# Optimization experiments

Hardware: AMD Instinct MI355X
Metric: run time of the kernel (lower is better)

## Reference

```python
import jax, jax.numpy as jnp
import numpy as np

D_IN = 1024
D_H = 1024

def setup_inputs() -> dict:
    key = jax.random.key(0)
    ks = jax.random.split(key, 9)
    s = 1.0 / np.sqrt(D_IN)
    inp = {
        'x': jax.random.normal(ks[0], (4, 2048, D_IN), dtype=jnp.float32),
        'wq': jax.random.uniform(ks[1], (D_IN, D_H), jnp.float32, -s, s),
        'bq': jax.random.uniform(ks[2], (D_H,), jnp.float32, -s, s),
        'wk': jax.random.uniform(ks[3], (D_IN, D_H), jnp.float32, -s, s),
        'bk': jax.random.uniform(ks[4], (D_H,), jnp.float32, -s, s),
        'wv': jax.random.uniform(ks[5], (D_IN, D_H), jnp.float32, -s, s),
        'bv': jax.random.uniform(ks[6], (D_H,), jnp.float32, -s, s),
        'wo': jax.random.uniform(ks[7], (D_H, D_IN), jnp.float32, -s, s),
        'bo': jax.random.uniform(ks[8], (D_IN,), jnp.float32, -s, s),
    }
    return inp

def reference(x, wq, bq, wk, bk, wv, bv, wo, bo):
    # q,k,v: [b, s, d]
    q = x @ wq + bq
    k = x @ wk + bk
    v = x @ wv + bv
    scale = 1.0 / jnp.sqrt(jnp.asarray(D_H, x.dtype))
    attn = jnp.einsum('bqd,bkd->bqk', q, k) * scale  # [b, s, s]
    attn = jax.nn.softmax(attn, axis=-1)
    score = jnp.einsum('bqk,bkd->bqd', attn, v)
    out = score @ wo + bo
    return out
```

## Files before the change

### kernel.cpp

```cpp
#include <hip/hip_runtime.h>


typedef unsigned short u16;
typedef short bf16x8 __attribute__((ext_vector_type(8)));
typedef float f32x4 __attribute__((ext_vector_type(4)));

#define SEQ 2048
#define DIM 1024

__device__ __forceinline__ u16 f2bf(float f) {
    unsigned u = __builtin_bit_cast(unsigned, f);
    u += 0x7fffu + ((u >> 16) & 1u);
    return (u16)(u >> 16);
}

__device__ __forceinline__ void async16(void* lds, const void* gmem) {
    __builtin_amdgcn_global_load_lds(
        (const __attribute__((address_space(1))) void*)gmem,
        (__attribute__((address_space(3))) void*)lds, 16, 0, 0);
}

__global__ __launch_bounds__(256) void cast_x_kernel(
    const float* __restrict__ x, u16* __restrict__ xb,
    const float* __restrict__ bq, const float* __restrict__ bk,
    const float* __restrict__ bv, float* __restrict__ bqkv,
    float* __restrict__ l)
{
    const int b = blockIdx.x;
    if (b < 8192) {
        const int idx = b * 256 + threadIdx.x;
        float4 v = ((const float4*)x)[idx];
        ushort4 o;
        o.x = f2bf(v.x); o.y = f2bf(v.y); o.z = f2bf(v.z); o.w = f2bf(v.w);
        ((ushort4*)xb)[idx] = o;
    } else {
        const int i = (b - 8192) * 256 + threadIdx.x;
        if (i < 3072)
            bqkv[i] = (i < 1024) ? bq[i] : (i < 2048) ? bk[i - 1024] : bv[i - 2048];
        else if (i < 3072 + 8192)
            l[i - 3072] = 0.f;
    }
}

__global__ __launch_bounds__(256) void transpose_cast_all(
    const float* __restrict__ W0, const float* __restrict__ W1,
    const float* __restrict__ W2, const float* __restrict__ W3,
    u16* __restrict__ Tqkv, u16* __restrict__ To)
{
    __shared__ float tile[32][33];
    const int z = blockIdx.z;
    const float* W = (z == 0) ? W0 : (z == 1) ? W1 : (z == 2) ? W2 : W3;
    u16* T = (z < 3) ? (Tqkv + (size_t)z * 1048576) : To;

    const int bx = blockIdx.x * 32, by = blockIdx.y * 32;
    const int tx = threadIdx.x, ty = threadIdx.y;
    #pragma unroll
    for (int r = 0; r < 4; ++r)
        tile[ty + r * 8][tx] = W[(size_t)(by + ty + r * 8) * DIM + bx + tx];
    __syncthreads();
    #pragma unroll
    for (int r = 0; r < 4; ++r) {
        const float v = tile[tx][ty + r * 8];
        T[(size_t)(bx + ty + r * 8) * DIM + by + tx] = f2bf(v);
    }
}

#define EPI_BF16BIAS 0
#define EPI_BF16     1
#define EPI_ELOGIT   2
#define EPI_PVOUT    3

#define FENCE() asm volatile("" ::: "memory")

#define MFMA_QUAD(mh, nh)                                                    \
    do {                                                                     \
        __builtin_amdgcn_s_setprio(1);                                       \
        _Pragma("unroll")                                                    \
        for (int ks = 0; ks < 2; ++ks)                                       \
            _Pragma("unroll")                                                \
            for (int q = 0; q < 4; ++q)                                      \
                _Pragma("unroll")                                            \
                for (int nn = 0; nn < 2; ++nn)                               \
                    acc[(mh) * 4 + q][(nh) * 2 + nn] =                       \
                        __builtin_amdgcn_mfma_f32_16x16x32_bf16(             \
                            aF[q][ks], bF[(nh) * 2 + nn][ks],                \
                            acc[(mh) * 4 + q][(nh) * 2 + nn], 0, 0, 0);      \
        __builtin_amdgcn_s_setprio(0);                                       \
    } while (0)

template<int EPI, int K, int LDA, int LDB, int LDC>
__global__ __launch_bounds__(512, 2) void gemm8w(
    const u16* __restrict__ A, const u16* __restrict__ Bt,
    const float* __restrict__ bias, u16* __restrict__ C,
    float* __restrict__ Cf, float* __restrict__ lsum,
    float scale, long sA, long sB, long sC)
{
    __shared__ u16 lds[2][2][2][8192];

    constexpr int NT = K / 64;

    const int z = blockIdx.z;
    A  += (size_t)z * sA;
    Bt += (size_t)z * sB;

    const int t = threadIdx.x;
    const int wid = t >> 6, lane = t & 63;
    const int wm = wid >> 2, wn = wid & 3;
    const int lrow = lane & 15, quad = lane >> 4;
    const int m0 = blockIdx.y * 256, n0 = blockIdx.x * 256;

    int ldsoff[2], offA[2], offB[2];
    #pragma unroll
    for (int p = 0; p < 2; ++p) {
        const int L  = p * 8192 + wid * 1024 + lane * 16;
        const int sL = L ^ (((L >> 7) & 7) << 4);
        const int r  = sL >> 7;
        const int c  = (sL & 127) >> 1;
        ldsoff[p] = L;
        offA[p]   = r * LDA + c;
        offB[p]   = r * LDB + c;
    }
    const u16* ABase = A  + (size_t)m0 * LDA;
    const u16* BBase = Bt + (size_t)n0 * LDB;

    auto stage = [&](int tile, int sel) {
        const int mat = sel >> 1, half = sel & 1, buf = tile & 1;
        char* dst = (char*)&lds[buf][mat][half][0];
        const int k0 = tile * 64;
        #pragma unroll
        for (int p = 0; p < 2; ++p) {
            const u16* src = mat
                ? BBase + (size_t)half * (128 * (size_t)LDB) + k0 + offB[p]
                : ABase + (size_t)half * (128 * (size_t)LDA) + k0 + offA[p];
            async16(dst + ldsoff[p], src);
        }
    };

    f32x4 acc[8][4];
    #pragma unroll
    for (int i = 0; i < 8; ++i)
        #pragma unroll
        for (int j = 0; j < 4; ++j)
            acc[i][j] = (f32x4){0.f, 0.f, 0.f, 0.f};

    bf16x8 aF[4][2], bF[4][2];

    auto ldA1 = [&](int buf, int mi, int ks) -> bf16x8 {
        int b = (mi * 16 + lrow) * 128 + ks * 64 + quad * 16;
        b ^= ((b >> 7) & 7) << 4;
        return *(const bf16x8*)((const char*)&lds[buf][0][wm][0] + b);
    };
    auto ldB1 = [&](int buf, int ni, int ks) -> bf16x8 {
        int b = ((wn & 1) * 64 + ni * 16 + lrow) * 128 + ks * 64 + quad * 16;
        b ^= ((b >> 7) & 7) << 4;
        return *(const bf16x8*)((const char*)&lds[buf][1][wn >> 1][0] + b);
    };

    stage(0, 0); stage(0, 1); stage(0, 2); stage(0, 3);
    stage(1, 2); stage(1, 3); stage(1, 0);
    asm volatile("s_waitcnt vmcnt(6)" ::: "memory");
    __builtin_amdgcn_s_barrier();

    #pragma unroll 1
    for (int T = 0; T < NT; ++T) {
        const int buf = T & 1;
        const bool s1 = (T + 1 < NT), s2 = (T + 2 < NT);

        #pragma unroll
        for (int q = 0; q < 4; ++q) {
            aF[q][0] = ldA1(buf, q, 0);
            aF[q][1] = ldA1(buf, q, 1);
        }
        #pragma unroll
        for (int ni = 0; ni < 4; ++ni) {
            bF[ni][0] = ldB1(buf, ni, 0);
            bF[ni][1] = ldB1(buf, ni, 1);
        }
        if (s1) stage(T + 1, 1);
        FENCE(); __builtin_amdgcn_s_barrier();
        MFMA_QUAD(0, 0);
        FENCE(); __builtin_amdgcn_s_barrier();

        MFMA_QUAD(0, 1);
        FENCE(); __builtin_amdgcn_s_barrier();

        #pragma unroll
        for (int q = 0; q < 4; ++q) {
            aF[q][0] = ldA1(buf, 4 + q, 0);
            aF[q][1] = ldA1(buf, 4 + q, 1);
        }
        if (s2) { stage(T + 2, 2); stage(T + 2, 3); }
        FENCE(); __builtin_amdgcn_s_barrier();
        MFMA_QUAD(1, 1);
        FENCE(); __builtin_amdgcn_s_barrier();

        if (s2) {
            stage(T + 2, 0);
            asm volatile("s_waitcnt vmcnt(6)" ::: "memory");
        } else {
            asm volatile("s_waitcnt vmcnt(0)" ::: "memory");
        }
        FENCE(); __builtin_amdgcn_s_barrier();
        MFMA_QUAD(1, 0);
        FENCE(); __builtin_amdgcn_s_barrier();
    }

    if (EPI == EPI_PVOUT) Cf += (size_t)z * sC;
    else                  C  += (size_t)z * sC;

    #pragma unroll
    for (int mi = 0; mi < 8; ++mi) {
        const int row = m0 + wm * 128 + mi * 16 + quad * 4;
        if (EPI == EPI_BF16BIAS) {
            #pragma unroll
            for (int ni = 0; ni < 4; ++ni) {
                const int col = n0 + wn * 64 + ni * 16 + lrow;
                const float bb = bias[col];
                const f32x4 a = acc[mi][ni];
                #pragma unroll
                for (int r = 0; r < 4; ++r)
                    C[(size_t)(row + r) * LDC + col] = f2bf(a[r] + bb);
            }
        } else if (EPI == EPI_BF16) {
            #pragma unroll
            for (int ni = 0; ni < 4; ++ni) {
                const int col = n0 + wn * 64 + ni * 16 + lrow;
                const f32x4 a = acc[mi][ni];
                #pragma unroll
                for (int r = 0; r < 4; ++r)
                    C[(size_t)(row + r) * LDC + col] = f2bf(a[r]);
            }
        } else if (EPI == EPI_ELOGIT) {
            float rs[4] = {0.f, 0.f, 0.f, 0.f};
            #pragma unroll
            for (int ni = 0; ni < 4; ++ni) {
                const int col = n0 + wn * 64 + ni * 16 + lrow;
                const f32x4 a = acc[mi][ni];
                #pragma unroll
                for (int r = 0; r < 4; ++r) {
                    const float e = __expf(a[r] * scale);
                    C[(size_t)(row + r) * LDC + col] = f2bf(e);
                    rs[r] += e;
                }
            }
            #pragma unroll
            for (int r = 0; r < 4; ++r) {
                float s = rs[r];
                s += __shfl_xor(s, 1, 64);
                s += __shfl_xor(s, 2, 64);
                s += __shfl_xor(s, 4, 64);
                s += __shfl_xor(s, 8, 64);
                if (lrow == 0)
                    atomicAdd(&lsum[(size_t)z * 2048 + row + r], s);
            }
        } else {
            float linv[4];
            #pragma unroll
            for (int r = 0; r < 4; ++r)
                linv[r] = 1.0f / lsum[(size_t)z * 2048 + row + r];
            #pragma unroll
            for (int ni = 0; ni < 4; ++ni) {
                const int col = n0 + wn * 64 + ni * 16 + lrow;
                const float bb = bias[col];
                const f32x4 a = acc[mi][ni];
                #pragma unroll
                for (int r = 0; r < 4; ++r)
                    Cf[(size_t)(row + r) * LDC + col] = a[r] * linv[r] + bb;
            }
        }
    }
}

extern "C" void kernel_launch(void* const* d_in, const int* in_sizes, int n_in,
                              void* d_out, int out_size, void* d_ws, size_t ws_size,
                              hipStream_t stream)
{
    const float* x  = (const float*)d_in[0];
    const float* wq = (const float*)d_in[1];
    const float* bq = (const float*)d_in[2];
    const float* wk = (const float*)d_in[3];
    const float* bk = (const float*)d_in[4];
    const float* wv = (const float*)d_in[5];
    const float* bv = (const float*)d_in[6];
    const float* wo = (const float*)d_in[7];
    const float* bo = (const float*)d_in[8];
    float* out = (float*)d_out;

    u16* w16   = (u16*)d_ws;
    u16* xb    = w16;
    u16* qkv   = w16 + 8388608;
    u16* E     = w16 + 33554432;
    u16* wqkvT = w16 + 50331648;
    u16* woT   = w16 + 53477376;
    float* bqkv = (float*)(w16 + 54525952);
    float* l    = (float*)(w16 + 54532096);
    u16* VWoT  = w16;

    const u16* q_ = qkv;
    const u16* k_ = qkv + 1024;
    const u16* v_ = qkv + 2048;

    cast_x_kernel<<<8236, dim3(256), 0, stream>>>(x, xb, bq, bk, bv, bqkv, l);
    transpose_cast_all<<<dim3(32, 32, 4), dim3(32, 8), 0, stream>>>(
        wq, wk, wv, wo, wqkvT, woT);

    gemm8w<EPI_BF16BIAS, 1024, 1024, 1024, 3072>
        <<<dim3(12, 32, 1), dim3(512), 0, stream>>>(
            xb, wqkvT, bqkv, qkv, nullptr, nullptr, 1.f, 0, 0, 0);

    gemm8w<EPI_ELOGIT, 1024, 3072, 3072, 2048>
        <<<dim3(8, 8, 4), dim3(512), 0, stream>>>(
            q_, k_, nullptr, E, nullptr, l, 0.03125f,
            6291456, 6291456, 4194304);

    gemm8w<EPI_BF16, 1024, 1024, 3072, 2048>
        <<<dim3(8, 4, 4), dim3(512), 0, stream>>>(
            woT, v_, nullptr, VWoT, nullptr, nullptr, 1.f,
            0, 6291456, 2097152);

    gemm8w<EPI_PVOUT, 2048, 2048, 2048, 1024>
        <<<dim3(4, 8, 4), dim3(512), 0, stream>>>(
            E, VWoT, bo, nullptr, out, l, 1.f,
            4194304, 2097152, 2097152);
}
```

Measured before the change: 304.0 us.

## Merge QK-logit and V·Wo GEMMs into one launch and split B-fragment loads

Turns the templated GEMM into one runtime-parameterised kernel that takes two argument structs and chooses between them by blockIdx.y. The QK^T-exp GEMM and the V·Wo GEMM now run in a single grid, which removes a launch and fills the GPU better, since the V·Wo GEMM alone had a small grid. The B-fragment LDS loads are also split, so the second half is loaded just before the MFMAs that use it, which lowers register pressure at the cost of an extra barrier. Leading dimensions and epilogue type become runtime values, so address arithmetic is no longer compile-time constant and the epilogue branches at runtime.

```diff
diff --git a/kernel.cpp b/kernel.cpp
--- a/kernel.cpp
+++ b/kernel.cpp
@@ -70,6 +70,14 @@
 #define EPI_ELOGIT   2
 #define EPI_PVOUT    3
 
+struct GArgs {
+    const u16* A; const u16* Bt; const float* bias;
+    u16* C; float* Cf; float* lsum;
+    float scale;
+    long sA, sB, sC;
+    int LDA, LDB, LDC, K, epi;
+};
+
 #define FENCE() asm volatile("" ::: "memory")
 
 #define MFMA_QUAD(mh, nh)                                                    \
@@ -88,26 +96,23 @@
         __builtin_amdgcn_s_setprio(0);                                       \
     } while (0)
 
-template<int EPI, int K, int LDA, int LDB, int LDC>
-__global__ __launch_bounds__(512, 2) void gemm8w(
-    const u16* __restrict__ A, const u16* __restrict__ Bt,
-    const float* __restrict__ bias, u16* __restrict__ C,
-    float* __restrict__ Cf, float* __restrict__ lsum,
-    float scale, long sA, long sB, long sC)
+__global__ __launch_bounds__(512, 2) void gemm8w(GArgs g0, GArgs g1, int ySplit)
 {
     __shared__ u16 lds[2][2][2][8192];
 
-    constexpr int NT = K / 64;
-
+    const int by = blockIdx.y;
+    GArgs g = g0;
+    int ty = by;
+    if (by >= ySplit) { g = g1; ty = by - ySplit; }
+
+    const int NT = g.K >> 6;
     const int z = blockIdx.z;
-    A  += (size_t)z * sA;
-    Bt += (size_t)z * sB;
 
     const int t = threadIdx.x;
     const int wid = t >> 6, lane = t & 63;
     const int wm = wid >> 2, wn = wid & 3;
     const int lrow = lane & 15, quad = lane >> 4;
-    const int m0 = blockIdx.y * 256, n0 = blockIdx.x * 256;
+    const int m0 = ty * 256, n0 = blockIdx.x * 256;
 
     int ldsoff[2], offA[2], offB[2];
     #pragma unroll
@@ -117,23 +122,21 @@
         const int r  = sL >> 7;
         const int c  = (sL & 127) >> 1;
         ldsoff[p] = L;
-        offA[p]   = r * LDA + c;
-        offB[p]   = r * LDB + c;
-    }
-    const u16* ABase = A  + (size_t)m0 * LDA;
-    const u16* BBase = Bt + (size_t)n0 * LDB;
+        offA[p]   = r * g.LDA + c;
+        offB[p]   = r * g.LDB + c;
+    }
+    const u16* ABase = g.A  + (size_t)z * g.sA + (size_t)m0 * g.LDA;
+    const u16* BBase = g.Bt + (size_t)z * g.sB + (size_t)n0 * g.LDB;
 
     auto stage = [&](int tile, int sel) {
         const int mat = sel >> 1, half = sel & 1, buf = tile & 1;
         char* dst = (char*)&lds[buf][mat][half][0];
         const int k0 = tile * 64;
-        #pragma unroll
-        for (int p = 0; p < 2; ++p) {
-            const u16* src = mat
-                ? BBase + (size_t)half * (128 * (size_t)LDB) + k0 + offB[p]
-                : ABase + (size_t)half * (128 * (size_t)LDA) + k0 + offA[p];
-            async16(dst + ldsoff[p], src);
-        }
+        const u16* base = mat ? BBase + (size_t)half * 128 * g.LDB
+                              : ABase + (size_t)half * 128 * g.LDA;
+        #pragma unroll
+        for (int p = 0; p < 2; ++p)
+            async16(dst + ldsoff[p], base + k0 + (mat ? offB[p] : offA[p]));
     };
 
     f32x4 acc[8][4];
@@ -172,7 +175,7 @@
             aF[q][1] = ldA1(buf, q, 1);
         }
         #pragma unroll
-        for (int ni = 0; ni < 4; ++ni) {
+        for (int ni = 0; ni < 2; ++ni) {
             bF[ni][0] = ldB1(buf, ni, 0);
             bF[ni][1] = ldB1(buf, ni, 1);
         }
@@ -181,6 +184,12 @@
         MFMA_QUAD(0, 0);
         FENCE(); __builtin_amdgcn_s_barrier();
 
+        #pragma unroll
+        for (int ni = 0; ni < 2; ++ni) {
+            bF[2 + ni][0] = ldB1(buf, 2 + ni, 0);
+            bF[2 + ni][1] = ldB1(buf, 2 + ni, 1);
+        }
+        FENCE(); __builtin_amdgcn_s_barrier();
         MFMA_QUAD(0, 1);
         FENCE(); __builtin_amdgcn_s_barrier();
 
@@ -205,32 +214,33 @@
         FENCE(); __builtin_amdgcn_s_barrier();
     }
 
-    if (EPI == EPI_PVOUT) Cf += (size_t)z * sC;
-    else                  C  += (size_t)z * sC;
+    const int epi = g.epi;
+    u16*   C  = g.C  ? g.C  + (size_t)z * g.sC : nullptr;
+    float* Cf = g.Cf ? g.Cf + (size_t)z * g.sC : nullptr;
 
     #pragma unroll
     for (int mi = 0; mi < 8; ++mi) {
         const int row = m0 + wm * 128 + mi * 16 + quad * 4;
-        if (EPI == EPI_BF16BIAS) {
+        if (epi == EPI_BF16BIAS) {
             #pragma unroll
             for (int ni = 0; ni < 4; ++ni) {
                 const int col = n0 + wn * 64 + ni * 16 + lrow;
-                const float bb = bias[col];
+                const float bb = g.bias[col];
                 const f32x4 a = acc[mi][ni];
                 #pragma unroll
                 for (int r = 0; r < 4; ++r)
-                    C[(size_t)(row + r) * LDC + col] = f2bf(a[r] + bb);
-            }
-        } else if (EPI == EPI_BF16) {
+                    C[(size_t)(row + r) * g.LDC + col] = f2bf(a[r] + bb);
+            }
+        } else if (epi == EPI_BF16) {
             #pragma unroll
             for (int ni = 0; ni < 4; ++ni) {
                 const int col = n0 + wn * 64 + ni * 16 + lrow;
                 const f32x4 a = acc[mi][ni];
                 #pragma unroll
                 for (int r = 0; r < 4; ++r)
-                    C[(size_t)(row + r) * LDC + col] = f2bf(a[r]);
-            }
-        } else if (EPI == EPI_ELOGIT) {
+                    C[(size_t)(row + r) * g.LDC + col] = f2bf(a[r]);
+            }
+        } else if (epi == EPI_ELOGIT) {
             float rs[4] = {0.f, 0.f, 0.f, 0.f};
             #pragma unroll
             for (int ni = 0; ni < 4; ++ni) {
@@ -238,8 +248,8 @@
                 const f32x4 a = acc[mi][ni];
                 #pragma unroll
                 for (int r = 0; r < 4; ++r) {
-                    const float e = __expf(a[r] * scale);
-                    C[(size_t)(row + r) * LDC + col] = f2bf(e);
+                    const float e = __expf(a[r] * g.scale);
+                    C[(size_t)(row + r) * g.LDC + col] = f2bf(e);
                     rs[r] += e;
                 }
             }
@@ -251,21 +261,21 @@
                 s += __shfl_xor(s, 4, 64);
                 s += __shfl_xor(s, 8, 64);
                 if (lrow == 0)
-                    atomicAdd(&lsum[(size_t)z * 2048 + row + r], s);
+                    atomicAdd(&g.lsum[(size_t)z * 2048 + row + r], s);
             }
         } else {
             float linv[4];
             #pragma unroll
             for (int r = 0; r < 4; ++r)
-                linv[r] = 1.0f / lsum[(size_t)z * 2048 + row + r];
+                linv[r] = 1.0f / g.lsum[(size_t)z * 2048 + row + r];
             #pragma unroll
             for (int ni = 0; ni < 4; ++ni) {
                 const int col = n0 + wn * 64 + ni * 16 + lrow;
-                const float bb = bias[col];
+                const float bb = g.bias[col];
                 const f32x4 a = acc[mi][ni];
                 #pragma unroll
                 for (int r = 0; r < 4; ++r)
-                    Cf[(size_t)(row + r) * LDC + col] = a[r] * linv[r] + bb;
+                    Cf[(size_t)(row + r) * g.LDC + col] = a[r] * linv[r] + bb;
             }
         }
     }
@@ -304,22 +314,14 @@
     transpose_cast_all<<<dim3(32, 32, 4), dim3(32, 8), 0, stream>>>(
         wq, wk, wv, wo, wqkvT, woT);
 
-    gemm8w<EPI_BF16BIAS, 1024, 1024, 1024, 3072>
-        <<<dim3(12, 32, 1), dim3(512), 0, stream>>>(
-            xb, wqkvT, bqkv, qkv, nullptr, nullptr, 1.f, 0, 0, 0);
-
-    gemm8w<EPI_ELOGIT, 1024, 3072, 3072, 2048>
-        <<<dim3(8, 8, 4), dim3(512), 0, stream>>>(
-            q_, k_, nullptr, E, nullptr, l, 0.03125f,
-            6291456, 6291456, 4194304);
-
-    gemm8w<EPI_BF16, 1024, 1024, 3072, 2048>
-        <<<dim3(8, 4, 4), dim3(512), 0, stream>>>(
-            woT, v_, nullptr, VWoT, nullptr, nullptr, 1.f,
-            0, 6291456, 2097152);
-
-    gemm8w<EPI_PVOUT, 2048, 2048, 2048, 1024>
-        <<<dim3(4, 8, 4), dim3(512), 0, stream>>>(
-            E, VWoT, bo, nullptr, out, l, 1.f,
-            4194304, 2097152, 2097152);
-}
+    GArgs gQKV{             xb,   wqkvT, bqkv,  qkv,  0,    0,    1.f,     0,       0,       0,      1024, 1024, 3072, 1024, EPI_BF16BIAS };
+    GArgs gQK {             q_,   k_,    0,     E,    0,    l,    0.03125f,6291456, 6291456, 4194304,3072, 3072, 2048, 1024, EPI_ELOGIT   };
+    GArgs gVW {             woT,  v_,    0,     VWoT, 0,    0,    1.f,     0,       6291456, 2097152,1024, 3072, 2048, 1024, EPI_BF16     };
+    GArgs gPV {             E,    VWoT,  bo,    0,    out,  l,    1.f,     4194304, 2097152, 2097152,2048, 2048, 1024, 2048, EPI_PVOUT    };
+
+    gemm8w<<<dim3(12, 32, 1), dim3(512), 0, stream>>>(gQKV, gQKV, 1 << 20);
+
+    gemm8w<<<dim3(8, 12, 4), dim3(512), 0, stream>>>(gQK, gVW, 8);
+
+    gemm8w<<<dim3(4, 8, 4), dim3(512), 0, stream>>>(gPV, gPV, 1 << 20);
+}
```

After: 308.9 us. About the same (+1.6%).

## Replace 256x256 8-wave GEMM with simpler 128x128 4-wave double-buffered GEMM

Applied to the files above, without the earlier changes.

Swaps the 8-wave 256x256 tile GEMM and its interleaved multi-barrier MFMA schedule for a 4-wave 128x128 tile kernel. The new kernel uses plain double buffering with one wait and barrier per K tile. All four GEMM launches get four times as many blocks. The aim is better occupancy and load balance across CUs, since the old grids were small (as few as 128 blocks). The cost is lower per-tile arithmetic intensity, more global and LDS traffic, and less overlap of loads with MFMA work.

```diff
diff --git a/kernel.cpp b/kernel.cpp
--- a/kernel.cpp
+++ b/kernel.cpp
@@ -19,6 +19,8 @@
         (const __attribute__((address_space(1))) void*)gmem,
         (__attribute__((address_space(3))) void*)lds, 16, 0, 0);
 }
+
+#define FENCE() asm volatile("" ::: "memory")
 
 __global__ __launch_bounds__(256) void cast_x_kernel(
     const float* __restrict__ x, u16* __restrict__ xb,
@@ -70,147 +72,107 @@
 #define EPI_ELOGIT   2
 #define EPI_PVOUT    3
 
-#define FENCE() asm volatile("" ::: "memory")
-
-#define MFMA_QUAD(mh, nh)                                                    \
-    do {                                                                     \
-        __builtin_amdgcn_s_setprio(1);                                       \
-        _Pragma("unroll")                                                    \
-        for (int ks = 0; ks < 2; ++ks)                                       \
-            _Pragma("unroll")                                                \
-            for (int q = 0; q < 4; ++q)                                      \
-                _Pragma("unroll")                                            \
-                for (int nn = 0; nn < 2; ++nn)                               \
-                    acc[(mh) * 4 + q][(nh) * 2 + nn] =                       \
-                        __builtin_amdgcn_mfma_f32_16x16x32_bf16(             \
-                            aF[q][ks], bF[(nh) * 2 + nn][ks],                \
-                            acc[(mh) * 4 + q][(nh) * 2 + nn], 0, 0, 0);      \
-        __builtin_amdgcn_s_setprio(0);                                       \
-    } while (0)
-
 template<int EPI, int K, int LDA, int LDB, int LDC>
-__global__ __launch_bounds__(512, 2) void gemm8w(
+__global__ __launch_bounds__(256, 2) void gemm4w(
     const u16* __restrict__ A, const u16* __restrict__ Bt,
     const float* __restrict__ bias, u16* __restrict__ C,
     float* __restrict__ Cf, float* __restrict__ lsum,
     float scale, long sA, long sB, long sC)
 {
-    __shared__ u16 lds[2][2][2][8192];
+    __shared__ u16 lds[2][2][8192];
 
     constexpr int NT = K / 64;
 
     const int z = blockIdx.z;
-    A  += (size_t)z * sA;
-    Bt += (size_t)z * sB;
-
     const int t = threadIdx.x;
     const int wid = t >> 6, lane = t & 63;
-    const int wm = wid >> 2, wn = wid & 3;
+    const int wm = wid >> 1, wn = wid & 1;
     const int lrow = lane & 15, quad = lane >> 4;
-    const int m0 = blockIdx.y * 256, n0 = blockIdx.x * 256;
-
-    int ldsoff[2], offA[2], offB[2];
-    #pragma unroll
-    for (int p = 0; p < 2; ++p) {
-        const int L  = p * 8192 + wid * 1024 + lane * 16;
-        const int sL = L ^ (((L >> 7) & 7) << 4);
-        const int r  = sL >> 7;
-        const int c  = (sL & 127) >> 1;
-        ldsoff[p] = L;
-        offA[p]   = r * LDA + c;
-        offB[p]   = r * LDB + c;
-    }
-    const u16* ABase = A  + (size_t)m0 * LDA;
-    const u16* BBase = Bt + (size_t)n0 * LDB;
-
-    auto stage = [&](int tile, int sel) {
-        const int mat = sel >> 1, half = sel & 1, buf = tile & 1;
-        char* dst = (char*)&lds[buf][mat][half][0];
+    const int m0 = blockIdx.y * 128, n0 = blockIdx.x * 128;
+
+    const u16* ABase = A  + (size_t)z * sA + (size_t)m0 * LDA;
+    const u16* BBase = Bt + (size_t)z * sB + (size_t)n0 * LDB;
+
+    int srow[4], scolOff[4];
+    #pragma unroll
+    for (int p = 0; p < 4; ++p) {
+        const int slot = p * 256 + t;
+        const int row  = slot >> 3;
+        const int c8   = (slot & 7) ^ (row & 7);
+        srow[p] = row; scolOff[p] = c8 * 8;
+    }
+
+    auto stage = [&](int tile, int buf) {
         const int k0 = tile * 64;
         #pragma unroll
-        for (int p = 0; p < 2; ++p) {
-            const u16* src = mat
-                ? BBase + (size_t)half * (128 * (size_t)LDB) + k0 + offB[p]
-                : ABase + (size_t)half * (128 * (size_t)LDA) + k0 + offA[p];
-            async16(dst + ldsoff[p], src);
+        for (int p = 0; p < 4; ++p) {
+            const int slot = p * 256 + t;
+            async16(&lds[buf][0][slot * 8],
+                    ABase + (size_t)srow[p] * LDA + k0 + scolOff[p]);
+        }
+        #pragma unroll
+        for (int p = 0; p < 4; ++p) {
+            const int slot = p * 256 + t;
+            async16(&lds[buf][1][slot * 8],
+                    BBase + (size_t)srow[p] * LDB + k0 + scolOff[p]);
         }
     };
 
-    f32x4 acc[8][4];
-    #pragma unroll
-    for (int i = 0; i < 8; ++i)
+    f32x4 acc[4][4];
+    #pragma unroll
+    for (int i = 0; i < 4; ++i)
         #pragma unroll
         for (int j = 0; j < 4; ++j)
             acc[i][j] = (f32x4){0.f, 0.f, 0.f, 0.f};
 
-    bf16x8 aF[4][2], bF[4][2];
-
     auto ldA1 = [&](int buf, int mi, int ks) -> bf16x8 {
-        int b = (mi * 16 + lrow) * 128 + ks * 64 + quad * 16;
+        int b = (wm * 64 + mi * 16 + lrow) * 128 + ks * 64 + quad * 16;
         b ^= ((b >> 7) & 7) << 4;
-        return *(const bf16x8*)((const char*)&lds[buf][0][wm][0] + b);
+        return *(const bf16x8*)((const char*)&lds[buf][0][0] + b);
     };
     auto ldB1 = [&](int buf, int ni, int ks) -> bf16x8 {
-        int b = ((wn & 1) * 64 + ni * 16 + lrow) * 128 + ks * 64 + quad * 16;
+        int b = (wn * 64 + ni * 16 + lrow) * 128 + ks * 64 + quad * 16;
         b ^= ((b >> 7) & 7) << 4;
-        return *(const bf16x8*)((const char*)&lds[buf][1][wn >> 1][0] + b);
+        return *(const bf16x8*)((const char*)&lds[buf][1][0] + b);
     };
 
-    stage(0, 0); stage(0, 1); stage(0, 2); stage(0, 3);
-    stage(1, 2); stage(1, 3); stage(1, 0);
-    asm volatile("s_waitcnt vmcnt(6)" ::: "memory");
-    __builtin_amdgcn_s_barrier();
+    stage(0, 0);
+    stage(1, 1);
 
     #pragma unroll 1
     for (int T = 0; T < NT; ++T) {
         const int buf = T & 1;
-        const bool s1 = (T + 1 < NT), s2 = (T + 2 < NT);
-
-        #pragma unroll
-        for (int q = 0; q < 4; ++q) {
-            aF[q][0] = ldA1(buf, q, 0);
-            aF[q][1] = ldA1(buf, q, 1);
-        }
-        #pragma unroll
-        for (int ni = 0; ni < 4; ++ni) {
-            bF[ni][0] = ldB1(buf, ni, 0);
-            bF[ni][1] = ldB1(buf, ni, 1);
-        }
-        if (s1) stage(T + 1, 1);
-        FENCE(); __builtin_amdgcn_s_barrier();
-        MFMA_QUAD(0, 0);
-        FENCE(); __builtin_amdgcn_s_barrier();
-
-        MFMA_QUAD(0, 1);
-        FENCE(); __builtin_amdgcn_s_barrier();
-
-        #pragma unroll
-        for (int q = 0; q < 4; ++q) {
-            aF[q][0] = ldA1(buf, 4 + q, 0);
-            aF[q][1] = ldA1(buf, 4 + q, 1);
-        }
-        if (s2) { stage(T + 2, 2); stage(T + 2, 3); }
-        FENCE(); __builtin_amdgcn_s_barrier();
-        MFMA_QUAD(1, 1);
-        FENCE(); __builtin_amdgcn_s_barrier();
-
-        if (s2) {
-            stage(T + 2, 0);
-            asm volatile("s_waitcnt vmcnt(6)" ::: "memory");
-        } else {
-            asm volatile("s_waitcnt vmcnt(0)" ::: "memory");
-        }
-        FENCE(); __builtin_amdgcn_s_barrier();
-        MFMA_QUAD(1, 0);
-        FENCE(); __builtin_amdgcn_s_barrier();
-    }
-
-    if (EPI == EPI_PVOUT) Cf += (size_t)z * sC;
-    else                  C  += (size_t)z * sC;
-
-    #pragma unroll
-    for (int mi = 0; mi < 8; ++mi) {
-        const int row = m0 + wm * 128 + mi * 16 + quad * 4;
+        if (T + 1 < NT) asm volatile("s_waitcnt vmcnt(8)" ::: "memory");
+        else            asm volatile("s_waitcnt vmcnt(0)" ::: "memory");
+        __builtin_amdgcn_s_barrier();
+
+        #pragma unroll
+        for (int ks = 0; ks < 2; ++ks) {
+            bf16x8 aF[4], bF[4];
+            #pragma unroll
+            for (int mi = 0; mi < 4; ++mi) aF[mi] = ldA1(buf, mi, ks);
+            #pragma unroll
+            for (int ni = 0; ni < 4; ++ni) bF[ni] = ldB1(buf, ni, ks);
+            __builtin_amdgcn_s_setprio(1);
+            #pragma unroll
+            for (int mi = 0; mi < 4; ++mi)
+                #pragma unroll
+                for (int ni = 0; ni < 4; ++ni)
+                    acc[mi][ni] = __builtin_amdgcn_mfma_f32_16x16x32_bf16(
+                        aF[mi], bF[ni], acc[mi][ni], 0, 0, 0);
+            __builtin_amdgcn_s_setprio(0);
+        }
+        FENCE();
+        __builtin_amdgcn_s_barrier();
+        if (T + 2 < NT) stage(T + 2, buf);
+    }
+
+    u16*   Cz  = C  + (size_t)z * sC;
+    float* Cfz = Cf ? Cf + (size_t)z * sC : nullptr;
+
+    #pragma unroll
+    for (int mi = 0; mi < 4; ++mi) {
+        const int row = m0 + wm * 64 + mi * 16 + quad * 4;
         if (EPI == EPI_BF16BIAS) {
             #pragma unroll
             for (int ni = 0; ni < 4; ++ni) {
@@ -219,7 +181,7 @@
                 const f32x4 a = acc[mi][ni];
                 #pragma unroll
                 for (int r = 0; r < 4; ++r)
-                    C[(size_t)(row + r) * LDC + col] = f2bf(a[r] + bb);
+                    Cz[(size_t)(row + r) * LDC + col] = f2bf(a[r] + bb);
             }
         } else if (EPI == EPI_BF16) {
             #pragma unroll
@@ -228,7 +190,7 @@
                 const f32x4 a = acc[mi][ni];
                 #pragma unroll
                 for (int r = 0; r < 4; ++r)
-                    C[(size_t)(row + r) * LDC + col] = f2bf(a[r]);
+                    Cz[(size_t)(row + r) * LDC + col] = f2bf(a[r]);
             }
         } else if (EPI == EPI_ELOGIT) {
             float rs[4] = {0.f, 0.f, 0.f, 0.f};
@@ -239,7 +201,7 @@
                 #pragma unroll
                 for (int r = 0; r < 4; ++r) {
                     const float e = __expf(a[r] * scale);
-                    C[(size_t)(row + r) * LDC + col] = f2bf(e);
+                    Cz[(size_t)(row + r) * LDC + col] = f2bf(e);
                     rs[r] += e;
                 }
             }
@@ -265,7 +227,7 @@
                 const f32x4 a = acc[mi][ni];
                 #pragma unroll
                 for (int r = 0; r < 4; ++r)
-                    Cf[(size_t)(row + r) * LDC + col] = a[r] * linv[r] + bb;
+                    Cfz[(size_t)(row + r) * LDC + col] = a[r] * linv[r] + bb;
             }
         }
     }
@@ -304,22 +266,22 @@
     transpose_cast_all<<<dim3(32, 32, 4), dim3(32, 8), 0, stream>>>(
         wq, wk, wv, wo, wqkvT, woT);
 
-    gemm8w<EPI_BF16BIAS, 1024, 1024, 1024, 3072>
-        <<<dim3(12, 32, 1), dim3(512), 0, stream>>>(
+    gemm4w<EPI_BF16BIAS, 1024, 1024, 1024, 3072>
+        <<<dim3(24, 64, 1), dim3(256), 0, stream>>>(
             xb, wqkvT, bqkv, qkv, nullptr, nullptr, 1.f, 0, 0, 0);
 
-    gemm8w<EPI_ELOGIT, 1024, 3072, 3072, 2048>
-        <<<dim3(8, 8, 4), dim3(512), 0, stream>>>(
+    gemm4w<EPI_ELOGIT, 1024, 3072, 3072, 2048>
+        <<<dim3(16, 16, 4), dim3(256), 0, stream>>>(
             q_, k_, nullptr, E, nullptr, l, 0.03125f,
             6291456, 6291456, 4194304);
 
-    gemm8w<EPI_BF16, 1024, 1024, 3072, 2048>
-        <<<dim3(8, 4, 4), dim3(512), 0, stream>>>(
+    gemm4w<EPI_BF16, 1024, 1024, 3072, 2048>
+        <<<dim3(16, 8, 4), dim3(256), 0, stream>>>(
             woT, v_, nullptr, VWoT, nullptr, nullptr, 1.f,
             0, 6291456, 2097152);
 
-    gemm8w<EPI_PVOUT, 2048, 2048, 2048, 1024>
-        <<<dim3(4, 8, 4), dim3(512), 0, stream>>>(
+    gemm4w<EPI_PVOUT, 2048, 2048, 2048, 1024>
+        <<<dim3(8, 16, 4), dim3(256), 0, stream>>>(
             E, VWoT, bo, nullptr, out, l, 1.f,
             4194304, 2097152, 2097152);
 }
```

Result: faster. 273.9 us (-9.9%).
